# Kernel tuning notes

Measured on AMD Instinct MI355X. Metric: run time of the kernel, lower is better.

Reference implementation:

```python
import jax, jax.numpy as jnp
import numpy as np

HIDDEN = 768
HEADS = 8
EXP = 4
EPS = 1e-5


def layer_norm(x, g, b):
    mu = jnp.mean(x, axis=-1, keepdims=True)
    var = jnp.mean(jnp.square(x - mu), axis=-1, keepdims=True)
    return (x - mu) * jax.lax.rsqrt(var + EPS) * g + b


def setup_inputs() -> dict:
    key = jax.random.key(0)
    ks = jax.random.split(key, 16)
    h, e = HIDDEN, EXP * HIDDEN
    s = 0.02
    return {
        "x": jax.random.normal(ks[0], (2, 4096, h), dtype=jnp.float32),
        "ln1_g": jnp.ones((h,), jnp.float32),
        "ln1_b": jnp.zeros((h,), jnp.float32),
        "wq": jax.random.normal(ks[1], (h, h), jnp.float32) * s,
        "bq": jnp.zeros((h,), jnp.float32),
        "wk": jax.random.normal(ks[2], (h, h), jnp.float32) * s,
        "bk": jnp.zeros((h,), jnp.float32),
        "wv": jax.random.normal(ks[3], (h, h), jnp.float32) * s,
        "bv": jnp.zeros((h,), jnp.float32),
        "wp": jax.random.normal(ks[4], (h, h), jnp.float32) * s,
        "bp": jnp.zeros((h,), jnp.float32),
        "ln2_g": jnp.ones((h,), jnp.float32),
        "ln2_b": jnp.zeros((h,), jnp.float32),
        "w1": jax.random.normal(ks[5], (h, e), jnp.float32) * s,
        "b1": jnp.zeros((e,), jnp.float32),
        "w2": jax.random.normal(ks[6], (e, h), jnp.float32) * s,
        "b2": jnp.zeros((h,), jnp.float32),
    }


def reference(x, ln1_g, ln1_b, wq, bq, wk, bk, wv, bv, wp, bp,
              ln2_g, ln2_b, w1, b1, w2, b2):
    n, s, h = x.shape
    d = h // HEADS

    # --- MSA branch (pre-LN) ---
    xn = layer_norm(x, ln1_g, ln1_b)
    q = (xn @ wq + bq).reshape(n, s, HEADS, d).transpose(0, 2, 1, 3)  # bhsd
    k = (xn @ wk + bk).reshape(n, s, HEADS, d).transpose(0, 2, 1, 3)
    v = (xn @ wv + bv).reshape(n, s, HEADS, d).transpose(0, 2, 1, 3)
    energy = jnp.einsum('bhqd,bhkd->bhqk', q, k)
    # faithful to original: softmax over the HEAD axis (dim=1), then scale
    att = jax.nn.softmax(energy, axis=1) / (h ** 0.5)
    attn_out = jnp.einsum('bhqk,bhkd->bhqd', att, v)
    attn_out = attn_out.transpose(0, 2, 1, 3).reshape(n, s, h)
    attn_out = attn_out @ wp + bp
    x = x + attn_out

    # --- MLP branch (pre-LN) ---
    xn = layer_norm(x, ln2_g, ln2_b)
    hmid = jax.nn.gelu(xn @ w1 + b1, approximate=False)
    x = x + (hmid @ w2 + b2)
    return x
```

## Files before the change

### kernel.cpp

```cpp
#include <hip/hip_runtime.h>
#include <cstdint>
#include <cstddef>

#define AS1 __attribute__((address_space(1)))
#define AS3 __attribute__((address_space(3)))

typedef __attribute__((ext_vector_type(8))) __bf16 bf16x8;
typedef __attribute__((ext_vector_type(4))) float f32x4;

__device__ __forceinline__ void gload_lds16(const void* g, void* l) {
  __builtin_amdgcn_global_load_lds((AS1 void*)g, (AS3 void*)l, 16, 0, 0);
}

__global__ void k_transpose_w(const float* __restrict__ src, __bf16* __restrict__ dst,
                              int K, int N, int ldd, int koff) {
  __shared__ float tile[32][33];
  const int bx = blockIdx.x * 32;
  const int by = blockIdx.y * 32;
  const int tx = threadIdx.x, ty = threadIdx.y;
#pragma unroll
  for (int ii = 0; ii < 4; ++ii) {
    int i = ty + ii * 8;
    tile[i][tx] = src[(size_t)(by + i) * N + bx + tx];
  }
  __syncthreads();
#pragma unroll
  for (int ii = 0; ii < 4; ++ii) {
    int i = ty + ii * 8;
    dst[(size_t)(bx + i) * ldd + koff + by + tx] = (__bf16)tile[tx][i];
  }
}

__global__ void k_pack_bias(const float* __restrict__ bq, const float* __restrict__ bk,
                            const float* __restrict__ bv, float* __restrict__ dst) {
  int i = blockIdx.x * 256 + threadIdx.x;
  if (i < 768) dst[i] = bq[i];
  else if (i < 1536) dst[i] = bk[i - 768];
  else if (i < 2304) dst[i] = bv[i - 1536];
}

__global__ __launch_bounds__(256) void k_layernorm(const float* __restrict__ x,
                                                   const float* __restrict__ g,
                                                   const float* __restrict__ b,
                                                   __bf16* __restrict__ out) {
  const int row = blockIdx.x * 4 + (threadIdx.x >> 6);
  const int lane = threadIdx.x & 63;
  const float* xr = x + (size_t)row * 768;
  float4 v[3];
#pragma unroll
  for (int j = 0; j < 3; ++j) v[j] = *(const float4*)(xr + j * 256 + lane * 4);
  float s = 0.f, ss = 0.f;
#pragma unroll
  for (int j = 0; j < 3; ++j) {
    s += v[j].x + v[j].y + v[j].z + v[j].w;
    ss += v[j].x * v[j].x + v[j].y * v[j].y + v[j].z * v[j].z + v[j].w * v[j].w;
  }
#pragma unroll
  for (int off = 32; off > 0; off >>= 1) {
    s += __shfl_xor(s, off);
    ss += __shfl_xor(ss, off);
  }
  const float mu = s * (1.f / 768.f);
  const float rstd = rsqrtf(ss * (1.f / 768.f) - mu * mu + 1e-5f);
  __bf16* orow = out + (size_t)row * 768;
#pragma unroll
  for (int j = 0; j < 3; ++j) {
    float4 gg = *(const float4*)(g + j * 256 + lane * 4);
    float4 bb = *(const float4*)(b + j * 256 + lane * 4);
    const int base = j * 256 + lane * 4;
    orow[base + 0] = (__bf16)((v[j].x - mu) * rstd * gg.x + bb.x);
    orow[base + 1] = (__bf16)((v[j].y - mu) * rstd * gg.y + bb.y);
    orow[base + 2] = (__bf16)((v[j].z - mu) * rstd * gg.z + bb.z);
    orow[base + 3] = (__bf16)((v[j].w - mu) * rstd * gg.w + bb.w);
  }
}

template <int MODE>
__global__ __launch_bounds__(256) void k_gemm(const __bf16* __restrict__ A,
                                              const __bf16* __restrict__ BT,
                                              const float* __restrict__ bias,
                                              const float* __restrict__ resid,
                                              void* __restrict__ Cout,
                                              int M, int N, int K, int lda, int ldb) {
  __shared__ __bf16 As[128 * 32];
  __shared__ __bf16 Bs[128 * 32];
  const int nx = N >> 7;
  const int rpx = (M >> 7) >> 3;
  const int xcd = blockIdx.x & 7;
  const int ib = blockIdx.x >> 3;
  const int n0 = (ib % nx) << 7;
  const int m0 = (xcd * rpx + ib / nx) << 7;
  if constexpr (MODE == 3) {
    A += (size_t)blockIdx.y * K;
    BT += (size_t)blockIdx.y * K;
  }
  const int tid = threadIdx.x;
  const int wid = tid >> 6, lane = tid & 63;
  const int wm = wid >> 1, wn = wid & 1;
  const int lr = lane & 15, lg = lane >> 4;

  f32x4 acc[4][4] = {};

  for (int k0 = 0; k0 < K; k0 += 32) {
#pragma unroll
    for (int it = 0; it < 2; ++it) {
      int t = tid + it * 256;
      int r = t >> 2, c = (t & 3) * 8;
      gload_lds16(A + (size_t)(m0 + r) * lda + k0 + c, As + t * 8);
      gload_lds16(BT + (size_t)(n0 + r) * ldb + k0 + c, Bs + t * 8);
    }
    __syncthreads();
    bf16x8 af[4], bf[4];
#pragma unroll
    for (int i = 0; i < 4; ++i) af[i] = *(const bf16x8*)(As + (wm * 64 + i * 16 + lr) * 32 + lg * 8);
#pragma unroll
    for (int j = 0; j < 4; ++j) bf[j] = *(const bf16x8*)(Bs + (wn * 64 + j * 16 + lr) * 32 + lg * 8);
#pragma unroll
    for (int i = 0; i < 4; ++i)
#pragma unroll
      for (int j = 0; j < 4; ++j)
        acc[i][j] = __builtin_amdgcn_mfma_f32_16x16x32_bf16(af[i], bf[j], acc[i][j], 0, 0, 0);
    __syncthreads();
  }

#pragma unroll
  for (int i = 0; i < 4; ++i)
#pragma unroll
    for (int j = 0; j < 4; ++j)
#pragma unroll
      for (int r = 0; r < 4; ++r) {
        int row = m0 + wm * 64 + i * 16 + lg * 4 + r;
        int col = n0 + wn * 64 + j * 16 + lr;
        float v = acc[i][j][r];
        if constexpr (MODE != 3) v += bias[col];
        size_t idx = (size_t)row * N + col;
        if constexpr (MODE == 0) {
          if (col < 768) v *= 1.44269504088896f;
          ((__bf16*)Cout)[idx] = (__bf16)v;
        } else if constexpr (MODE == 1) {
          ((float*)Cout)[idx] = v + resid[idx];
        } else if constexpr (MODE == 2) {
          float u = 0.7978845608f * (v + 0.044715f * v * v * v);
          float t = __builtin_amdgcn_exp2f(u * 2.88539008f);
          float th = 1.f - 2.f * __builtin_amdgcn_rcpf(t + 1.f);
          ((__bf16*)Cout)[idx] = (__bf16)(0.5f * v * (1.f + th));
        } else {
          ((__bf16*)Cout)[(size_t)blockIdx.y * M * N + idx] = (__bf16)v;
        }
      }
}

__global__ __launch_bounds__(256) void k_fuse_mlp2(const __bf16* __restrict__ p0,
                                                   const __bf16* __restrict__ p1,
                                                   const float* __restrict__ bias,
                                                   const float* __restrict__ resid,
                                                   float* __restrict__ out) {
  int g = blockIdx.x * 256 + threadIdx.x;
  int base = g * 8;
  int col = base % 768;
  bf16x8 a = *(const bf16x8*)(p0 + base);
  bf16x8 b = *(const bf16x8*)(p1 + base);
  float4 r0 = *(const float4*)(resid + base);
  float4 r1 = *(const float4*)(resid + base + 4);
  float4 b0 = *(const float4*)(bias + col);
  float4 b1 = *(const float4*)(bias + col + 4);
  float4 o0, o1;
  o0.x = r0.x + b0.x + (float)a[0] + (float)b[0];
  o0.y = r0.y + b0.y + (float)a[1] + (float)b[1];
  o0.z = r0.z + b0.z + (float)a[2] + (float)b[2];
  o0.w = r0.w + b0.w + (float)a[3] + (float)b[3];
  o1.x = r1.x + b1.x + (float)a[4] + (float)b[4];
  o1.y = r1.y + b1.y + (float)a[5] + (float)b[5];
  o1.z = r1.z + b1.z + (float)a[6] + (float)b[6];
  o1.w = r1.w + b1.w + (float)a[7] + (float)b[7];
  *(float4*)(out + base) = o0;
  *(float4*)(out + base + 4) = o1;
}

__global__ __launch_bounds__(256) void k_pack_ka(const __bf16* __restrict__ qkv,
                                                 __bf16* __restrict__ KA) {
  const int kb = blockIdx.x, b = blockIdx.y;
  const int t = threadIdx.x;
#pragma unroll
  for (int i = 0; i < 6; ++i) {
    int c = t + i * 256;
    int lane = c & 63, f = c >> 6;
    int dc = f % 3, hh = (f / 3) & 1, hp = f / 6;
    int row = kb * 16 + (lane & 15);
    int col = 768 + hp * 192 + hh * 96 + dc * 32 + (lane >> 4) * 8;
    bf16x8 v = *(const bf16x8*)(qkv + (size_t)(b * 4096 + row) * 2304 + col);
    *(bf16x8*)(KA + ((size_t)(b * 256 + kb) * 1536 + c) * 8) = v;
  }
}

__global__ __launch_bounds__(256) void k_pack_va(const __bf16* __restrict__ qkv,
                                                 __bf16* __restrict__ VA) {
  __shared__ __bf16 vtile[32][772];
  const int g = blockIdx.x, b = blockIdx.y;
  const int t = threadIdx.x;
#pragma unroll
  for (int i = 0; i < 12; ++i) {
    int c = t + i * 256;
    int row = c / 96, c8 = c % 96;
    *(bf16x8*)(&vtile[row][c8 * 8]) =
        *(const bf16x8*)(qkv + (size_t)(b * 4096 + g * 32 + row) * 2304 + 1536 + c8 * 8);
  }
  __syncthreads();
#pragma unroll
  for (int i = 0; i < 12; ++i) {
    int c = t + i * 256;
    int lane = c & 63, f = c >> 6;
    int db = f % 6, hh = (f / 6) & 1, hp = f / 12;
    int d = hp * 192 + hh * 96 + db * 16 + (lane & 15);
    int lg_ = lane >> 4;
    bf16x8 v;
#pragma unroll
    for (int e = 0; e < 8; ++e) {
      int krow = (e >> 2) * 16 + lg_ * 4 + (e & 3);
      v[e] = vtile[krow][d];
    }
    *(bf16x8*)(VA + ((size_t)(b * 128 + g) * 3072 + c) * 8) = v;
  }
}

__global__ __launch_bounds__(1024, 4) void k_attn(const __bf16* __restrict__ qkv,
                                                  const __bf16* __restrict__ KA,
                                                  const __bf16* __restrict__ VA,
                                                  __bf16* __restrict__ attn4) {
  __shared__ __bf16 Kb_s[2][12288];
  __shared__ __bf16 Vb_s[24576];
  __shared__ float ps_s[2][4352];
  const int bid = blockIdx.x;
  const int slice = bid & 7;
  const int b = slice >> 2, ks = slice & 3;
  const int qb = bid >> 3;
  const int wid = threadIdx.x >> 6;
  const int qs = wid & 3, hp = wid >> 2;
  const int q0 = qb * 64 + qs * 16;
  const int lane = threadIdx.x & 63;
  const int lr = lane & 15, lg = lane >> 4;

  const __bf16* Qb = qkv + (size_t)(b * 4096 + q0) * 2304;
  bf16x8 qf[2][3];
#pragma unroll
  for (int hh = 0; hh < 2; ++hh)
#pragma unroll
    for (int dc = 0; dc < 3; ++dc)
      qf[hh][dc] = *(const bf16x8*)(Qb + (size_t)lr * 2304 + (hp * 2 + hh) * 96 + dc * 32 + lg * 8);

  const int L1 = wid, hpK1 = L1 / 6, jK1 = L1 - hpK1 * 6;
  const int L2 = wid + 16, hpK2 = L2 / 6, jK2 = L2 - hpK2 * 6;

  int kb = ks * 64;
  {
    const __bf16* srcK = KA + (size_t)(b * 256 + kb) * 12288;
    gload_lds16(srcK + hpK1 * 3072 + jK1 * 512 + lane * 8,
                &Kb_s[0][hpK1 * 3072 + jK1 * 512 + lane * 8]);
    if (wid < 8)
      gload_lds16(srcK + hpK2 * 3072 + jK2 * 512 + lane * 8,
                  &Kb_s[0][hpK2 * 3072 + jK2 * 512 + lane * 8]);
  }
  asm volatile("s_waitcnt vmcnt(0)" ::: "memory");
  __builtin_amdgcn_s_barrier();
  asm volatile("" ::: "memory");

  f32x4 o[2][6] = {};
  f32x4 eA[2], eB[2];

#define HALF(ET, PAR, DO_V, DO_PV) do {                                               \
    {                      \
      size_t kidx = (size_t)(b * 256 + kb + 1);                                       \
      if (kidx > 511) kidx = 511;                                                     \
      const __bf16* srcK = KA + kidx * 12288;                                         \
      gload_lds16(srcK + hpK1 * 3072 + jK1 * 512 + lane * 8,                          \
                  &Kb_s[PAR ^ 1][hpK1 * 3072 + jK1 * 512 + lane * 8]);                \
      if (wid < 8)                                                                    \
        gload_lds16(srcK + hpK2 * 3072 + jK2 * 512 + lane * 8,                        \
                    &Kb_s[PAR ^ 1][hpK2 * 3072 + jK2 * 512 + lane * 8]);              \
    }                                                                                 \
    if (DO_V) {     \
      const __bf16* srcV = VA + (size_t)(b * 128 + (kb >> 1)) * 24576;                \
      _Pragma("unroll")                                                               \
      for (int tt = 0; tt < 3; ++tt) {                                                \
        int L = wid * 3 + tt;                                                         \
        int hpV = L / 12, jV = L - hpV * 12;                                          \
        gload_lds16(srcV + hpV * 6144 + jV * 512 + lane * 8,                          \
                    &Vb_s[hpV * 6144 + jV * 512 + lane * 8]);                         \
      }                                                                               \
    }                                                                                 \
                                                                   \
    ET[0] = (f32x4){0.f, 0.f, 0.f, 0.f};                                              \
    ET[1] = (f32x4){0.f, 0.f, 0.f, 0.f};                                              \
    {                                                                                 \
      const __bf16* kbase = &Kb_s[PAR][hp * 3072 + lane * 8];                         \
      __builtin_amdgcn_s_setprio(1);                                                  \
      _Pragma("unroll")                                                               \
      for (int hh = 0; hh < 2; ++hh)                                                  \
        _Pragma("unroll")                                                             \
        for (int dc = 0; dc < 3; ++dc) {                                              \
          bf16x8 kf = *(const bf16x8*)(kbase + (hh * 3 + dc) * 512);                  \
          ET[hh] = __builtin_amdgcn_mfma_f32_16x16x32_bf16(kf, qf[hh][dc], ET[hh],    \
                                                           0, 0, 0);                  \
        }                                                                             \
      __builtin_amdgcn_s_setprio(0);                                                  \
    }                                                                                 \
              \
    _Pragma("unroll")                                                                 \
    for (int rr = 0; rr < 4; ++rr) {                                                  \
      float e0 = __builtin_amdgcn_exp2f(ET[0][rr]);                                   \
      float e1 = __builtin_amdgcn_exp2f(ET[1][rr]);                                   \
      ET[0][rr] = e0;                                                                 \
      ET[1][rr] = e1;                                                                 \
      ps_s[PAR][qs * 1088 + (lg * 4 + rr) * 68 + hp * 17 + lr] = e0 + e1;             \
    }                                                                                 \
    if (DO_V) {                                                                       \
      asm volatile("s_waitcnt vmcnt(3) lgkmcnt(0)" ::: "memory");                     \
    } else {                                                                          \
      asm volatile("s_waitcnt vmcnt(0) lgkmcnt(0)" ::: "memory");                     \
    }                                                                                 \
    __builtin_amdgcn_s_barrier();                                                     \
    asm volatile("" ::: "memory");                                                    \
                                    \
    {                                                                                 \
      float inv_[4];                                                                  \
      _Pragma("unroll")                                                               \
      for (int rr = 0; rr < 4; ++rr) {                                                \
        const int base = qs * 1088 + (lg * 4 + rr) * 68 + lr;                         \
        float tot = (ps_s[PAR][base] + ps_s[PAR][base + 17]) +                        \
                    (ps_s[PAR][base + 34] + ps_s[PAR][base + 51]);                    \
        inv_[rr] = 0.03608439182435161f * __builtin_amdgcn_rcpf(tot);                 \
      }                                                                               \
      _Pragma("unroll")                                                               \
      for (int rr = 0; rr < 4; ++rr) {                                                \
        ET[0][rr] *= inv_[rr];                                                        \
        ET[1][rr] *= inv_[rr];                                                        \
      }                                                                               \
    }                                                                                 \
    if (DO_PV) {            \
      bf16x8 pf0, pf1;                                                                \
      _Pragma("unroll")                                                               \
      for (int e2 = 0; e2 < 8; ++e2) {                                                \
        int rr = e2 & 3;                                                              \
        if (e2 < 4) { pf0[e2] = (__bf16)eA[0][rr]; pf1[e2] = (__bf16)eA[1][rr]; }     \
        else        { pf0[e2] = (__bf16)eB[0][rr]; pf1[e2] = (__bf16)eB[1][rr]; }     \
      }                                                                               \
      const __bf16* vbase = &Vb_s[hp * 6144 + lane * 8];                              \
      __builtin_amdgcn_s_setprio(1);                                                  \
      _Pragma("unroll")                                                               \
      for (int db = 0; db < 6; ++db) {                                                \
        bf16x8 vf0 = *(const bf16x8*)(vbase + db * 512);                              \
        bf16x8 vf1 = *(const bf16x8*)(vbase + (6 + db) * 512);                        \
        o[0][db] = __builtin_amdgcn_mfma_f32_16x16x32_bf16(pf0, vf0, o[0][db], 0, 0, 0); \
        o[1][db] = __builtin_amdgcn_mfma_f32_16x16x32_bf16(pf1, vf1, o[1][db], 0, 0, 0); \
      }                                                                               \
      __builtin_amdgcn_s_setprio(0);                                                  \
    }                                                                                 \
    ++kb;                                                                             \
  } while (0)

  for (int rp = 0; rp < 64; rp += 2) {
    HALF(eA, 0, 1, 0);
    HALF(eB, 1, 0, 1);
  }
#undef HALF

#pragma unroll
  for (int hh = 0; hh < 2; ++hh)
#pragma unroll
    for (int db = 0; db < 6; ++db)
#pragma unroll
      for (int rr = 0; rr < 4; ++rr)
        attn4[(size_t)(b * 4096 + q0 + lg * 4 + rr) * 3072 + ks * 768 +
              (hp * 2 + hh) * 96 + db * 16 + lr] = (__bf16)o[hh][db][rr];
}

__global__ __launch_bounds__(256) void k_reduce_attn(const __bf16* __restrict__ attn4,
                                                     __bf16* __restrict__ out) {
  int g = blockIdx.x * 256 + threadIdx.x;
  int row = g / 96, c8 = g % 96;
  const __bf16* p = attn4 + (size_t)row * 3072 + c8 * 8;
  float acc[8] = {};
#pragma unroll
  for (int s = 0; s < 4; ++s) {
    bf16x8 v = *(const bf16x8*)(p + s * 768);
#pragma unroll
    for (int e = 0; e < 8; ++e) acc[e] += (float)v[e];
  }
  bf16x8 r;
#pragma unroll
  for (int e = 0; e < 8; ++e) r[e] = (__bf16)acc[e];
  *(bf16x8*)(out + (size_t)row * 768 + c8 * 8) = r;
}

extern "C" void kernel_launch(void* const* d_in, const int* in_sizes, int n_in,
                              void* d_out, int out_size, void* d_ws, size_t ws_size,
                              hipStream_t stream) {
  (void)in_sizes; (void)n_in; (void)out_size; (void)ws_size;
  const float* x     = (const float*)d_in[0];
  const float* ln1_g = (const float*)d_in[1];
  const float* ln1_b = (const float*)d_in[2];
  const float* wq    = (const float*)d_in[3];
  const float* bq    = (const float*)d_in[4];
  const float* wk    = (const float*)d_in[5];
  const float* bk    = (const float*)d_in[6];
  const float* wv    = (const float*)d_in[7];
  const float* bv    = (const float*)d_in[8];
  const float* wp    = (const float*)d_in[9];
  const float* bp    = (const float*)d_in[10];
  const float* ln2_g = (const float*)d_in[11];
  const float* ln2_b = (const float*)d_in[12];
  const float* w1    = (const float*)d_in[13];
  const float* b1    = (const float*)d_in[14];
  const float* w2    = (const float*)d_in[15];
  const float* b2    = (const float*)d_in[16];

  char* ws = (char*)d_ws;
  const size_t o_wqkvT = 0;
  const size_t o_wpT   = o_wqkvT + (size_t)2304 * 768 * 2;
  const size_t o_w1T   = o_wpT   + (size_t)768 * 768 * 2;
  const size_t o_w2T   = o_w1T   + (size_t)768 * 3072 * 2;
  const size_t o_bqkv  = o_w2T   + (size_t)3072 * 768 * 2;
  const size_t o_xn    = o_bqkv  + (size_t)2304 * 4;
  const size_t o_qkv   = o_xn    + (size_t)8192 * 768 * 2;
  const size_t o_KA    = o_qkv   + (size_t)8192 * 2304 * 2;
  const size_t o_VA    = o_KA    + (size_t)2 * 256 * 1536 * 8 * 2;
  const size_t o_attn4 = o_VA    + (size_t)2 * 128 * 3072 * 8 * 2;
  const size_t o_x1      = o_attn4;
  const size_t o_part    = o_attn4 + (size_t)8192 * 768 * 4;
  const size_t o_attnred = o_KA;
  const size_t o_xn2     = o_VA;
  const size_t o_hmid    = o_xn;

  __bf16* wqkvT = (__bf16*)(ws + o_wqkvT);
  __bf16* wpT   = (__bf16*)(ws + o_wpT);
  __bf16* w1T   = (__bf16*)(ws + o_w1T);
  __bf16* w2T   = (__bf16*)(ws + o_w2T);
  float*  bqkv  = (float*)(ws + o_bqkv);
  __bf16* xn    = (__bf16*)(ws + o_xn);
  __bf16* qkvb  = (__bf16*)(ws + o_qkv);
  __bf16* KA    = (__bf16*)(ws + o_KA);
  __bf16* VA    = (__bf16*)(ws + o_VA);
  __bf16* attn4 = (__bf16*)(ws + o_attn4);
  float*  x1    = (float*)(ws + o_x1);
  __bf16* part  = (__bf16*)(ws + o_part);
  __bf16* attnr = (__bf16*)(ws + o_attnred);
  __bf16* xn2   = (__bf16*)(ws + o_xn2);
  __bf16* hmid  = (__bf16*)(ws + o_hmid);

  dim3 tb(32, 8);
  k_transpose_w<<<dim3(24, 24), tb, 0, stream>>>(wq, wqkvT, 768, 768, 768, 0);
  k_transpose_w<<<dim3(24, 24), tb, 0, stream>>>(wk, wqkvT + (size_t)768 * 768, 768, 768, 768, 0);
  k_transpose_w<<<dim3(24, 24), tb, 0, stream>>>(wv, wqkvT + (size_t)2 * 768 * 768, 768, 768, 768, 0);
  k_transpose_w<<<dim3(24, 24), tb, 0, stream>>>(wp, wpT, 768, 768, 768, 0);
  k_transpose_w<<<dim3(96, 24), tb, 0, stream>>>(w1, w1T, 768, 3072, 768, 0);
  k_transpose_w<<<dim3(24, 96), tb, 0, stream>>>(w2, w2T, 3072, 768, 3072, 0);
  k_pack_bias<<<9, 256, 0, stream>>>(bq, bk, bv, bqkv);

  k_layernorm<<<2048, 256, 0, stream>>>(x, ln1_g, ln1_b, xn);
  k_gemm<0><<<1152, 256, 0, stream>>>(xn, wqkvT, bqkv, nullptr, qkvb, 8192, 2304, 768, 768, 768);
  k_pack_ka<<<dim3(256, 2), 256, 0, stream>>>(qkvb, KA);
  k_pack_va<<<dim3(128, 2), 256, 0, stream>>>(qkvb, VA);
  k_attn<<<512, 1024, 0, stream>>>(qkvb, KA, VA, attn4);
  k_reduce_attn<<<3072, 256, 0, stream>>>(attn4, attnr);
  k_gemm<1><<<384, 256, 0, stream>>>(attnr, wpT, bp, x, x1, 8192, 768, 768, 768, 768);
  k_layernorm<<<2048, 256, 0, stream>>>(x1, ln2_g, ln2_b, xn2);
  k_gemm<2><<<1536, 256, 0, stream>>>(xn2, w1T, b1, nullptr, hmid, 8192, 3072, 768, 768, 768);
  k_gemm<3><<<dim3(384, 2), 256, 0, stream>>>(hmid, w2T, nullptr, nullptr, part,
                                              8192, 768, 1536, 3072, 3072);
  k_fuse_mlp2<<<3072, 256, 0, stream>>>(part, part + (size_t)8192 * 768, b2, x1,
                                        (float*)d_out);
}
```

Before: 469.9 us.

## Halve attention key-split, fuse K/V packing and batch weight transposes

The attention kernel now splits the key range 2 ways instead of 4, so it launches 256 blocks that each loop over twice as many key blocks. The partial output buffer and the reduction kernel shrink to match. Separately, the K and V packing kernels are merged into one launch, and the four 768x768 weight transposes run as a single 3D-grid launch. The goal is less partial-output traffic and reduction work plus fewer launches, at the cost of fewer, longer attention blocks and less parallelism to hide latency.

```diff
diff --git a/kernel.cpp b/kernel.cpp
--- a/kernel.cpp
+++ b/kernel.cpp
@@ -28,6 +28,34 @@
   for (int ii = 0; ii < 4; ++ii) {
     int i = ty + ii * 8;
     dst[(size_t)(bx + i) * ldd + koff + by + tx] = (__bf16)tile[tx][i];
+  }
+}
+
+__global__ void k_transpose_w4(const float* __restrict__ s0, const float* __restrict__ s1,
+                               const float* __restrict__ s2, const float* __restrict__ s3,
+                               __bf16* __restrict__ d0, __bf16* __restrict__ d1,
+                               __bf16* __restrict__ d2, __bf16* __restrict__ d3) {
+  __shared__ float tile[32][33];
+  const float* src;
+  __bf16* dst;
+  switch (blockIdx.z) {
+    case 0: src = s0; dst = d0; break;
+    case 1: src = s1; dst = d1; break;
+    case 2: src = s2; dst = d2; break;
+    default: src = s3; dst = d3; break;
+  }
+  const int bx = blockIdx.x * 32, by = blockIdx.y * 32;
+  const int tx = threadIdx.x, ty = threadIdx.y;
+#pragma unroll
+  for (int ii = 0; ii < 4; ++ii) {
+    int i = ty + ii * 8;
+    tile[i][tx] = src[(size_t)(by + i) * 768 + bx + tx];
+  }
+  __syncthreads();
+#pragma unroll
+  for (int ii = 0; ii < 4; ++ii) {
+    int i = ty + ii * 8;
+    dst[(size_t)(bx + i) * 768 + by + tx] = (__bf16)tile[tx][i];
   }
 }
 
@@ -177,27 +205,26 @@
   *(float4*)(out + base + 4) = o1;
 }
 
-__global__ __launch_bounds__(256) void k_pack_ka(const __bf16* __restrict__ qkv,
-                                                 __bf16* __restrict__ KA) {
-  const int kb = blockIdx.x, b = blockIdx.y;
-  const int t = threadIdx.x;
-#pragma unroll
-  for (int i = 0; i < 6; ++i) {
-    int c = t + i * 256;
-    int lane = c & 63, f = c >> 6;
-    int dc = f % 3, hh = (f / 3) & 1, hp = f / 6;
-    int row = kb * 16 + (lane & 15);
-    int col = 768 + hp * 192 + hh * 96 + dc * 32 + (lane >> 4) * 8;
-    bf16x8 v = *(const bf16x8*)(qkv + (size_t)(b * 4096 + row) * 2304 + col);
-    *(bf16x8*)(KA + ((size_t)(b * 256 + kb) * 1536 + c) * 8) = v;
-  }
-}
-
-__global__ __launch_bounds__(256) void k_pack_va(const __bf16* __restrict__ qkv,
+__global__ __launch_bounds__(256) void k_pack_kv(const __bf16* __restrict__ qkv,
+                                                 __bf16* __restrict__ KA,
                                                  __bf16* __restrict__ VA) {
   __shared__ __bf16 vtile[32][772];
   const int g = blockIdx.x, b = blockIdx.y;
   const int t = threadIdx.x;
+#pragma unroll
+  for (int half = 0; half < 2; ++half) {
+    int kb = g * 2 + half;
+#pragma unroll
+    for (int i = 0; i < 6; ++i) {
+      int c = t + i * 256;
+      int lane = c & 63, f = c >> 6;
+      int dc = f % 3, hh = (f / 3) & 1, hp = f / 6;
+      int row = kb * 16 + (lane & 15);
+      int col = 768 + hp * 192 + hh * 96 + dc * 32 + (lane >> 4) * 8;
+      bf16x8 v = *(const bf16x8*)(qkv + (size_t)(b * 4096 + row) * 2304 + col);
+      *(bf16x8*)(KA + ((size_t)(b * 256 + kb) * 1536 + c) * 8) = v;
+    }
+  }
 #pragma unroll
   for (int i = 0; i < 12; ++i) {
     int c = t + i * 256;
@@ -226,14 +253,14 @@
 __global__ __launch_bounds__(1024, 4) void k_attn(const __bf16* __restrict__ qkv,
                                                   const __bf16* __restrict__ KA,
                                                   const __bf16* __restrict__ VA,
-                                                  __bf16* __restrict__ attn4) {
+                                                  __bf16* __restrict__ attn2) {
   __shared__ __bf16 Kb_s[2][12288];
   __shared__ __bf16 Vb_s[24576];
   __shared__ float ps_s[2][4352];
   const int bid = blockIdx.x;
-  const int slice = bid & 7;
-  const int b = slice >> 2, ks = slice & 3;
-  const int qb = bid >> 3;
+  const int slice = bid & 3;
+  const int b = slice >> 1, ks = slice & 1;
+  const int qb = bid >> 2;
   const int wid = threadIdx.x >> 6;
   const int qs = wid & 3, hp = wid >> 2;
   const int q0 = qb * 64 + qs * 16;
@@ -251,7 +278,7 @@
   const int L1 = wid, hpK1 = L1 / 6, jK1 = L1 - hpK1 * 6;
   const int L2 = wid + 16, hpK2 = L2 / 6, jK2 = L2 - hpK2 * 6;
 
-  int kb = ks * 64;
+  int kb = ks * 128;
   {
     const __bf16* srcK = KA + (size_t)(b * 256 + kb) * 12288;
     gload_lds16(srcK + hpK1 * 3072 + jK1 * 512 + lane * 8,
@@ -270,7 +297,8 @@
 #define HALF(ET, PAR, DO_V, DO_PV) do {                                               \
     {                      \
       size_t kidx = (size_t)(b * 256 + kb + 1);                                       \
-      if (kidx > 511) kidx = 511;                                                     \
+      size_t kmax = (size_t)(b * 256 + 255);                                          \
+      if (kidx > kmax) kidx = kmax;                                                   \
       const __bf16* srcK = KA + kidx * 12288;                                         \
       gload_lds16(srcK + hpK1 * 3072 + jK1 * 512 + lane * 8,                          \
                   &Kb_s[PAR ^ 1][hpK1 * 3072 + jK1 * 512 + lane * 8]);                \
@@ -288,7 +316,6 @@
                     &Vb_s[hpV * 6144 + jV * 512 + lane * 8]);                         \
       }                                                                               \
     }                                                                                 \
-                                                                   \
     ET[0] = (f32x4){0.f, 0.f, 0.f, 0.f};                                              \
     ET[1] = (f32x4){0.f, 0.f, 0.f, 0.f};                                              \
     {                                                                                 \
@@ -304,7 +331,6 @@
         }                                                                             \
       __builtin_amdgcn_s_setprio(0);                                                  \
     }                                                                                 \
-              \
     _Pragma("unroll")                                                                 \
     for (int rr = 0; rr < 4; ++rr) {                                                  \
       float e0 = __builtin_amdgcn_exp2f(ET[0][rr]);                                   \
@@ -320,7 +346,6 @@
     }                                                                                 \
     __builtin_amdgcn_s_barrier();                                                     \
     asm volatile("" ::: "memory");                                                    \
-                                    \
     {                                                                                 \
       float inv_[4];                                                                  \
       _Pragma("unroll")                                                               \
@@ -336,7 +361,7 @@
         ET[1][rr] *= inv_[rr];                                                        \
       }                                                                               \
     }                                                                                 \
-    if (DO_PV) {            \
+    if (DO_PV) {                                                                      \
       bf16x8 pf0, pf1;                                                                \
       _Pragma("unroll")                                                               \
       for (int e2 = 0; e2 < 8; ++e2) {                                                \
@@ -358,7 +383,7 @@
     ++kb;                                                                             \
   } while (0)
 
-  for (int rp = 0; rp < 64; rp += 2) {
+  for (int rp = 0; rp < 128; rp += 2) {
     HALF(eA, 0, 1, 0);
     HALF(eB, 1, 0, 1);
   }
@@ -370,25 +395,20 @@
     for (int db = 0; db < 6; ++db)
 #pragma unroll
       for (int rr = 0; rr < 4; ++rr)
-        attn4[(size_t)(b * 4096 + q0 + lg * 4 + rr) * 3072 + ks * 768 +
+        attn2[(size_t)(b * 4096 + q0 + lg * 4 + rr) * 1536 + ks * 768 +
               (hp * 2 + hh) * 96 + db * 16 + lr] = (__bf16)o[hh][db][rr];
 }
 
-__global__ __launch_bounds__(256) void k_reduce_attn(const __bf16* __restrict__ attn4,
+__global__ __launch_bounds__(256) void k_reduce_attn(const __bf16* __restrict__ attn2,
                                                      __bf16* __restrict__ out) {
   int g = blockIdx.x * 256 + threadIdx.x;
   int row = g / 96, c8 = g % 96;
-  const __bf16* p = attn4 + (size_t)row * 3072 + c8 * 8;
-  float acc[8] = {};
-#pragma unroll
-  for (int s = 0; s < 4; ++s) {
-    bf16x8 v = *(const bf16x8*)(p + s * 768);
-#pragma unroll
-    for (int e = 0; e < 8; ++e) acc[e] += (float)v[e];
-  }
+  const __bf16* p = attn2 + (size_t)row * 1536 + c8 * 8;
+  bf16x8 v0 = *(const bf16x8*)(p);
+  bf16x8 v1 = *(const bf16x8*)(p + 768);
   bf16x8 r;
 #pragma unroll
-  for (int e = 0; e < 8; ++e) r[e] = (__bf16)acc[e];
+  for (int e = 0; e < 8; ++e) r[e] = (__bf16)((float)v0[e] + (float)v1[e]);
   *(bf16x8*)(out + (size_t)row * 768 + c8 * 8) = r;
 }
 
@@ -424,9 +444,9 @@
   const size_t o_qkv   = o_xn    + (size_t)8192 * 768 * 2;
   const size_t o_KA    = o_qkv   + (size_t)8192 * 2304 * 2;
   const size_t o_VA    = o_KA    + (size_t)2 * 256 * 1536 * 8 * 2;
-  const size_t o_attn4 = o_VA    + (size_t)2 * 128 * 3072 * 8 * 2;
-  const size_t o_x1      = o_attn4;
-  const size_t o_part    = o_attn4 + (size_t)8192 * 768 * 4;
+  const size_t o_attn2 = o_VA    + (size_t)2 * 128 * 3072 * 8 * 2;
+  const size_t o_x1      = o_attn2;
+  const size_t o_part    = o_attn2 + (size_t)8192 * 768 * 4;
   const size_t o_attnred = o_KA;
   const size_t o_xn2     = o_VA;
   const size_t o_hmid    = o_xn;
@@ -440,7 +460,7 @@
   __bf16* qkvb  = (__bf16*)(ws + o_qkv);
   __bf16* KA    = (__bf16*)(ws + o_KA);
   __bf16* VA    = (__bf16*)(ws + o_VA);
-  __bf16* attn4 = (__bf16*)(ws + o_attn4);
+  __bf16* attn2 = (__bf16*)(ws + o_attn2);
   float*  x1    = (float*)(ws + o_x1);
   __bf16* part  = (__bf16*)(ws + o_part);
   __bf16* attnr = (__bf16*)(ws + o_attnred);
@@ -448,20 +468,18 @@
   __bf16* hmid  = (__bf16*)(ws + o_hmid);
 
   dim3 tb(32, 8);
-  k_transpose_w<<<dim3(24, 24), tb, 0, stream>>>(wq, wqkvT, 768, 768, 768, 0);
-  k_transpose_w<<<dim3(24, 24), tb, 0, stream>>>(wk, wqkvT + (size_t)768 * 768, 768, 768, 768, 0);
-  k_transpose_w<<<dim3(24, 24), tb, 0, stream>>>(wv, wqkvT + (size_t)2 * 768 * 768, 768, 768, 768, 0);
-  k_transpose_w<<<dim3(24, 24), tb, 0, stream>>>(wp, wpT, 768, 768, 768, 0);
+  k_transpose_w4<<<dim3(24, 24, 4), tb, 0, stream>>>(wq, wk, wv, wp,
+                                                     wqkvT, wqkvT + (size_t)768 * 768,
+                                                     wqkvT + (size_t)2 * 768 * 768, wpT);
   k_transpose_w<<<dim3(96, 24), tb, 0, stream>>>(w1, w1T, 768, 3072, 768, 0);
   k_transpose_w<<<dim3(24, 96), tb, 0, stream>>>(w2, w2T, 3072, 768, 3072, 0);
   k_pack_bias<<<9, 256, 0, stream>>>(bq, bk, bv, bqkv);
 
   k_layernorm<<<2048, 256, 0, stream>>>(x, ln1_g, ln1_b, xn);
   k_gemm<0><<<1152, 256, 0, stream>>>(xn, wqkvT, bqkv, nullptr, qkvb, 8192, 2304, 768, 768, 768);
-  k_pack_ka<<<dim3(256, 2), 256, 0, stream>>>(qkvb, KA);
-  k_pack_va<<<dim3(128, 2), 256, 0, stream>>>(qkvb, VA);
-  k_attn<<<512, 1024, 0, stream>>>(qkvb, KA, VA, attn4);
-  k_reduce_attn<<<3072, 256, 0, stream>>>(attn4, attnr);
+  k_pack_kv<<<dim3(128, 2), 256, 0, stream>>>(qkvb, KA, VA);
+  k_attn<<<256, 1024, 0, stream>>>(qkvb, KA, VA, attn2);
+  k_reduce_attn<<<3072, 256, 0, stream>>>(attn2, attnr);
   k_gemm<1><<<384, 256, 0, stream>>>(attnr, wpT, bp, x, x1, 8192, 768, 768, 768, 768);
   k_layernorm<<<2048, 256, 0, stream>>>(x1, ln2_g, ln2_b, xn2);
   k_gemm<2><<<1536, 256, 0, stream>>>(xn2, w1T, b1, nullptr, hmid, 8192, 3072, 768, 768, 768);
```

Measured after the change: 445.9 us. 5.1% less time.
